# Performance work log

Hardware: AMD Instinct MI355X
Metric: run time of the kernel (lower is better)

Reference implementation:

```python
import jax, jax.numpy as jnp
import numpy as np

VOCAB = 50000
D = 256        # embedding_dim = nb_head * size_per_head
H = 8          # nb_head
DH = 32        # size_per_head
B = 8192
L = 64


def setup_inputs() -> dict:
    key = jax.random.key(0)
    ks = jax.random.split(key, 8)
    tokens = jax.random.randint(ks[0], (B, L), 0, VOCAB)
    scale = 0.02
    emb_table = jax.random.normal(ks[1], (VOCAB, D), dtype=jnp.float32) * scale
    WQ = jax.random.normal(ks[2], (D, D), dtype=jnp.float32) * scale
    WK = jax.random.normal(ks[3], (D, D), dtype=jnp.float32) * scale
    WV = jax.random.normal(ks[4], (D, D), dtype=jnp.float32) * scale
    WO = jax.random.normal(ks[5], (D, D), dtype=jnp.float32) * scale
    dense_w = jax.random.normal(ks[6], (D, 1), dtype=jnp.float32) * scale
    dense_b = jnp.zeros((1,), dtype=jnp.float32)
    return {"tokens": tokens, "emb_table": emb_table, "WQ": WQ, "WK": WK,
            "WV": WV, "WO": WO, "dense_w": dense_w, "dense_b": dense_b}


def _fastformer(x, WQ, WK, WV, WO):
    # x: [B, L, D]
    b, l, _ = x.shape
    Q = (x @ WQ).reshape(b, l, H, DH)
    K = (x @ WK).reshape(b, l, H, DH)
    V = (x @ WV).reshape(b, l, H, DH)
    global_q = jnp.mean(Q, axis=1, keepdims=True)   # [B,1,H,DH]
    global_k = jnp.mean(K, axis=1, keepdims=True)
    w = jnp.sum(global_q * K + global_k * Q, axis=-1)  # [B,L,H]
    w = jax.nn.softmax(w, axis=1)                       # softmax over seq
    context = (w[..., None] * V).reshape(b, l, D)
    return context @ WO


def reference(tokens, emb_table, WQ, WK, WV, WO, dense_w, dense_b):
    # NewsEncoder forward (inference: dropout = identity; masks computed but
    # unused by Fastformer.call, matching the original code).
    title_emb = emb_table[tokens]                       # [B,L,D]
    hidden = _fastformer(title_emb, WQ, WK, WV, WO)     # [B,L,D]
    scores = (hidden @ dense_w + dense_b)[..., 0]       # [B,L]
    attn = jax.nn.softmax(scores, axis=1)               # over seq
    news_vector = jnp.sum(hidden * attn[..., None], axis=1)  # [B,D]
    return news_vector
```

## Files before the change

### kernel.cpp

```cpp
#include <hip/hip_runtime.h>
#include <cstdint>


using f32x4  = __attribute__((ext_vector_type(4))) float;
using bf16x8 = __attribute__((ext_vector_type(8))) short;

__device__ __forceinline__ unsigned int pack2bf(float a, float b) {
  unsigned int ua = __builtin_bit_cast(unsigned int, a);
  unsigned int ub = __builtin_bit_cast(unsigned int, b);
  ua = (ua + 0x7fffu + ((ua >> 16) & 1u)) >> 16;
  ub = (ub + 0x7fffu + ((ub >> 16) & 1u)) >> 16;
  return ua | (ub << 16);
}
__device__ __forceinline__ unsigned short bf1(float a) {
  unsigned int ua = __builtin_bit_cast(unsigned int, a);
  ua = (ua + 0x7fffu + ((ua >> 16) & 1u)) >> 16;
  return (unsigned short)ua;
}
__device__ __forceinline__ float ubf(unsigned int u) {
  return __builtin_bit_cast(float, u << 16);
}
__device__ __forceinline__ void gload_lds16(const void* g, void* l) {
  __builtin_amdgcn_global_load_lds(
      (const __attribute__((address_space(1))) void*)g,
      (__attribute__((address_space(3))) void*)l, 16, 0, 0);
}

__global__ __launch_bounds__(256) void prep_all(const float* __restrict__ WQ,
                                                const float* __restrict__ WK,
                                                const float* __restrict__ WV,
                                                const float* __restrict__ WO,
                                                const float* __restrict__ dw,
                                                unsigned short* __restrict__ mbf,
                                                unsigned short* __restrict__ tkn,
                                                unsigned short* __restrict__ ptb) {
  const int t = threadIdx.x;
  const int bid = blockIdx.x;
  if (bid == 0) {
    __shared__ float wod[256];
    float acc = 0.f;
    for (int e = 0; e < 256; e += 4) {
      const float4 w4 = *(const float4*)(WO + (size_t)t * 256 + e);
      const float4 d4 = *(const float4*)(dw + e);
      acc += w4.x * d4.x + w4.y * d4.y + w4.z * d4.z + w4.w * d4.w;
    }
    wod[t] = acc;
    __syncthreads();
    for (int h = 0; h < 8; ++h) {
      float a = 0.f;
      for (int j = 0; j < 32; j += 4) {
        const float4 w4 = *(const float4*)(WV + (size_t)t * 256 + h * 32 + j);
        a += w4.x * wod[h*32+j] + w4.y * wod[h*32+j+1] + w4.z * wod[h*32+j+2] + w4.w * wod[h*32+j+3];
      }
      const float o = __shfl_xor(a, 1);
      if (!(t & 1)) ((unsigned int*)mbf)[h * 128 + (t >> 1)] = pack2bf(a, o);
    }
  } else if (bid <= 256) {
    __shared__ float ek[8][32], eq[8][32];
    const int n0 = (bid - 1) * 8;
    const int h  = n0 >> 8;
    {
      const int ei = t >> 5, j = t & 31;
      const int e = (n0 & 255) + ei;
      ek[ei][j] = WK[(size_t)e * 256 + h * 32 + j];
      eq[ei][j] = WQ[(size_t)e * 256 + h * 32 + j];
    }
    __syncthreads();
    float wqd[32], wkd[32];
#pragma unroll
    for (int j = 0; j < 32; j += 4) {
      *(float4*)(wqd + j) = *(const float4*)(WQ + (size_t)t * 256 + h * 32 + j);
      *(float4*)(wkd + j) = *(const float4*)(WK + (size_t)t * 256 + h * 32 + j);
    }
#pragma unroll
    for (int ei = 0; ei < 8; ++ei) {
      float a = 0.f;
#pragma unroll
      for (int j = 0; j < 32; ++j) a += wqd[j] * ek[ei][j] + wkd[j] * eq[ei][j];
      const float o = __shfl_xor(a, 1);
      if (!(t & 1)) ((unsigned int*)tkn)[(size_t)(n0 + ei) * 128 + (t >> 1)] = pack2bf(a, o);
    }
  } else {
    __shared__ float wvs[32][32];
    __shared__ float wos[32][256];
    const int pb = bid - 257;
    const int h = pb >> 3, d0 = (pb & 7) * 32;
    {
      const int dd = t >> 3, jq = (t & 7) * 4;
      *(float4*)(&wvs[dd][jq]) = *(const float4*)(WV + (size_t)(d0 + dd) * 256 + h * 32 + jq);
      const int c4 = (t & 63) * 4;
#pragma unroll
      for (int jj = 0; jj < 8; ++jj) {
        const int j = (t >> 6) * 8 + jj;
        *(float4*)(&wos[j][c4]) = *(const float4*)(WO + (size_t)(h * 32 + j) * 256 + c4);
      }
    }
    __syncthreads();
    const int n = t;
#pragma unroll 4
    for (int dd = 0; dd < 32; ++dd) {
      float a = 0.f;
#pragma unroll
      for (int j = 0; j < 32; ++j) a += wvs[dd][j] * wos[j][n];
      ptb[(size_t)n * 2048 + h * 256 + d0 + dd] = bf1(a);
    }
  }
}

__global__ __launch_bounds__(256) void ebf_kernel(const float4* __restrict__ emb4,
                                                  uint2* __restrict__ out2, int n) {
  for (int i = blockIdx.x * 256 + threadIdx.x; i < n; i += gridDim.x * 256) {
    const float4 v = emb4[i];
    uint2 pk;
    pk.x = pack2bf(v.x, v.y);
    pk.y = pack2bf(v.z, v.w);
    out2[i] = pk;
  }
}

__global__ __launch_bounds__(256) void xbar_kernel(const int* __restrict__ tokens,
                                                   const unsigned short* __restrict__ ebf,
                                                   unsigned short* __restrict__ xbf) {
  __shared__ int tok[64];
  __shared__ float part[8][256];
  const int b = blockIdx.x, t = threadIdx.x;
  if (t < 64) tok[t] = tokens[b * 64 + t];
  __syncthreads();
  const int rg = t >> 5;
  const int c16 = t & 31;
  const uint4* e4 = (const uint4*)ebf;
  float s[8] = {};
#pragma unroll
  for (int ri = 0; ri < 8; ++ri) {
    const uint4 u = e4[(size_t)tok[rg * 8 + ri] * 32 + c16];
    s[0] += ubf(u.x & 0xffffu); s[1] += ubf(u.x >> 16);
    s[2] += ubf(u.y & 0xffffu); s[3] += ubf(u.y >> 16);
    s[4] += ubf(u.z & 0xffffu); s[5] += ubf(u.z >> 16);
    s[6] += ubf(u.w & 0xffffu); s[7] += ubf(u.w >> 16);
  }
#pragma unroll
  for (int j = 0; j < 8; ++j) part[rg][c16 * 8 + j] = s[j];
  __syncthreads();
  float a = 0.f;
#pragma unroll
  for (int rg2 = 0; rg2 < 8; ++rg2) a += part[rg2][t];
  a *= (1.f / 64.f);
  const float o = __shfl_xor(a, 1);
  if (!(t & 1)) ((unsigned int*)xbf)[(size_t)b * 128 + (t >> 1)] = pack2bf(a, o);
}

__global__ __launch_bounds__(256) void cgemm(const unsigned short* __restrict__ xbf,
                                             const unsigned short* __restrict__ tkn,
                                             unsigned short* __restrict__ cbf) {
  __shared__ unsigned short As[64 * 264];
  const int t = threadIdx.x;
  const int m0 = blockIdx.x * 64, n0 = blockIdx.y * 64;
#pragma unroll
  for (int it = 0; it < 8; ++it) {
    const int idx = it * 256 + t;
    const int row = idx >> 5, c = idx & 31;
    const uint4 v = *(const uint4*)(xbf + (size_t)(m0 + row) * 256 + c * 8);
    *(uint4*)(As + row * 264 + c * 8) = v;
  }
  __syncthreads();
  const int wv = t >> 6, l = t & 63;
  const int g = l >> 4, r = l & 15;
#pragma unroll
  for (int nt = 0; nt < 4; ++nt) {
    const int n = n0 + nt * 16 + r;
    f32x4 acc = {0.f, 0.f, 0.f, 0.f};
#pragma unroll
    for (int kk = 0; kk < 8; ++kk) {
      const bf16x8 a  = *(const bf16x8*)(As + (16 * wv + r) * 264 + kk * 32 + g * 8);
      const bf16x8 bb = *(const bf16x8*)(tkn + (size_t)n * 256 + kk * 32 + g * 8);
      acc = __builtin_amdgcn_mfma_f32_16x16x32_bf16(a, bb, acc, 0, 0, 0);
    }
#pragma unroll
    for (int i = 0; i < 4; ++i)
      cbf[(size_t)(m0 + 16 * wv + g * 4 + i) * 2048 + n] = bf1(acc[i]);
  }
}

__global__ __launch_bounds__(256) void main_kernel(const int* __restrict__ tokens,
                                                   const unsigned short* __restrict__ ebf,
                                                   const unsigned short* __restrict__ mbf,
                                                   const float* __restrict__ dense_b,
                                                   unsigned short* __restrict__ cbf) {
  __shared__ unsigned short xl[64 * 256];
  __shared__ float wslds[64 * 17];
  __shared__ unsigned short cfT[16 * 80];
  const int t = threadIdx.x;
  const int b = blockIdx.x;
  const int wv = t >> 6, l = t & 63;
  const int g = l >> 4, r = l & 15;
  {
    unsigned int* cz = (unsigned int*)(cfT + 8 * 80);
    for (int z = t; z < 320; z += 256) cz[z] = 0u;
  }
  {
    const int ln = t & 63;
#pragma unroll
    for (int it = 0; it < 8; ++it) {
      const int R0 = it * 8 + wv * 2;
      const int R  = R0 + (ln >> 5);
      const int j  = ln & 31;
      const int tk = tokens[b * 64 + R];
      const int swzR = (R & 7) ^ (R >> 3);
      const unsigned short* src = ebf + (size_t)tk * 256 + ((j ^ swzR) << 3);
      gload_lds16(src, (void*)(xl + R0 * 256));
    }
  }
  __syncthreads();
  {
    const unsigned short* arow = xl + (16 * wv + r) * 256;
    const int sw = (r & 7) ^ ((2 * wv + (r >> 3)) & 7);
    const unsigned short* brow = (r < 8) ? (cbf + (size_t)b * 2048 + r * 256)
                                         : (mbf + (size_t)(r - 8) * 256);
    f32x4 acc = {0.f, 0.f, 0.f, 0.f};
#pragma unroll
    for (int kk = 0; kk < 8; ++kk) {
      const bf16x8 a  = *(const bf16x8*)(arow + (((kk * 4 + g) ^ sw) << 3));
      const bf16x8 bb = *(const bf16x8*)(brow + kk * 32 + g * 8);
      acc = __builtin_amdgcn_mfma_f32_16x16x32_bf16(a, bb, acc, 0, 0, 0);
    }
#pragma unroll
    for (int i = 0; i < 4; ++i)
      wslds[(16 * wv + g * 4 + i) * 17 + r] = acc[i];
  }
  __syncthreads();
  {
#pragma unroll
    for (int hh = 0; hh < 2; ++hh) {
      const int h = 2 * wv + hh;
      const float v = wslds[l * 17 + h];
      float mx = v;
#pragma unroll
      for (int sft = 32; sft; sft >>= 1) mx = fmaxf(mx, __shfl_xor(mx, sft));
      const float e = expf(v - mx);
      float sm = e;
#pragma unroll
      for (int sft = 32; sft; sft >>= 1) sm += __shfl_xor(sm, sft);
      wslds[l * 17 + h] = e / sm;
    }
  }
  __syncthreads();
  {
    float p[8], sv[8];
#pragma unroll
    for (int h = 0; h < 8; ++h) { p[h] = wslds[l*17 + h]; sv[h] = wslds[l*17 + 8 + h]; }
    float sc = dense_b[0];
#pragma unroll
    for (int h = 0; h < 8; ++h) sc += p[h] * sv[h];
    float mx = sc;
#pragma unroll
    for (int sft = 32; sft; sft >>= 1) mx = fmaxf(mx, __shfl_xor(mx, sft));
    const float e = expf(sc - mx);
    float sm = e;
#pragma unroll
    for (int sft = 32; sft; sft >>= 1) sm += __shfl_xor(sm, sft);
    const float attn = e / sm;
    float cc0, cc1;
    if      (wv == 0) { cc0 = attn * p[0]; cc1 = attn * p[1]; }
    else if (wv == 1) { cc0 = attn * p[2]; cc1 = attn * p[3]; }
    else if (wv == 2) { cc0 = attn * p[4]; cc1 = attn * p[5]; }
    else              { cc0 = attn * p[6]; cc1 = attn * p[7]; }
    cfT[(2 * wv) * 80 + l]     = bf1(cc0);
    cfT[(2 * wv + 1) * 80 + l] = bf1(cc1);
  }
  __syncthreads();
  {
    const bf16x8 a0 = *(const bf16x8*)(cfT + r * 80 + g * 8);
    const bf16x8 a1 = *(const bf16x8*)(cfT + r * 80 + 32 + g * 8);
    const short* xs = (const short*)xl;
#pragma unroll
    for (int nt = 0; nt < 4; ++nt) {
      const int d = wv * 64 + nt * 16 + r;
      short bv0[8], bv1[8];
#pragma unroll
      for (int j = 0; j < 8; ++j) {
        const int c0 = ((d >> 3) ^ j ^ g) << 3;
        bv0[j] = xs[(g * 8 + j) * 256 + (c0 | (d & 7))];
        const int c1 = ((d >> 3) ^ j ^ g ^ 4) << 3;
        bv1[j] = xs[(32 + g * 8 + j) * 256 + (c1 | (d & 7))];
      }
      f32x4 acc = {0.f, 0.f, 0.f, 0.f};
      acc = __builtin_amdgcn_mfma_f32_16x16x32_bf16(a0, *(const bf16x8*)bv0, acc, 0, 0, 0);
      acc = __builtin_amdgcn_mfma_f32_16x16x32_bf16(a1, *(const bf16x8*)bv1, acc, 0, 0, 0);
      if (g < 2) {
#pragma unroll
        for (int i = 0; i < 4; ++i) {
          const int h = g * 4 + i;
          cbf[(size_t)b * 2048 + h * 256 + d] = bf1(acc[i]);
        }
      }
    }
  }
}

__global__ __launch_bounds__(256) void pgemm(const unsigned short* __restrict__ cbf,
                                             const unsigned short* __restrict__ ptb,
                                             float* __restrict__ out) {
  __shared__ unsigned short As[32 * 264];
  const int t = threadIdx.x;
  const int m0 = blockIdx.x * 32, n0 = blockIdx.y * 64;
  const int wv = t >> 6, l = t & 63;
  const int g = l >> 4, r = l & 15;
  const int msub = wv & 1, nhalf = wv >> 1;
  f32x4 acc[2] = {};
  for (int kc = 0; kc < 8; ++kc) {
    __syncthreads();
#pragma unroll
    for (int it = 0; it < 4; ++it) {
      const int idx = it * 256 + t;
      const int row = idx >> 5, c = idx & 31;
      const uint4 v = *(const uint4*)(cbf + (size_t)(m0 + row) * 2048 + kc * 256 + c * 8);
      *(uint4*)(As + row * 264 + c * 8) = v;
    }
    __syncthreads();
#pragma unroll
    for (int kk = 0; kk < 8; ++kk) {
      const bf16x8 a = *(const bf16x8*)(As + (16 * msub + r) * 264 + kk * 32 + g * 8);
#pragma unroll
      for (int nt = 0; nt < 2; ++nt) {
        const int n = n0 + (nhalf * 2 + nt) * 16 + r;
        const bf16x8 bb = *(const bf16x8*)(ptb + (size_t)n * 2048 + kc * 256 + kk * 32 + g * 8);
        acc[nt] = __builtin_amdgcn_mfma_f32_16x16x32_bf16(a, bb, acc[nt], 0, 0, 0);
      }
    }
  }
#pragma unroll
  for (int nt = 0; nt < 2; ++nt) {
    const int n = n0 + (nhalf * 2 + nt) * 16 + r;
#pragma unroll
    for (int i = 0; i < 4; ++i)
      out[(size_t)(m0 + 16 * msub + g * 4 + i) * 256 + n] = acc[nt][i];
  }
}

extern "C" void kernel_launch(void* const* d_in, const int* in_sizes, int n_in,
                              void* d_out, int out_size, void* d_ws, size_t ws_size,
                              hipStream_t stream) {
  const int*   tokens = (const int*)d_in[0];
  const float* emb    = (const float*)d_in[1];
  const float* WQ     = (const float*)d_in[2];
  const float* WK     = (const float*)d_in[3];
  const float* WV     = (const float*)d_in[4];
  const float* WO     = (const float*)d_in[5];
  const float* dw     = (const float*)d_in[6];
  const float* db     = (const float*)d_in[7];
  float* out = (float*)d_out;

  unsigned short* base = (unsigned short*)d_ws;
  unsigned short* mbf  = base;
  unsigned short* xbf  = base + 2048;
  unsigned short* tkn  = xbf + (size_t)8192 * 256;
  unsigned short* cbf  = tkn + (size_t)2048 * 256;
  unsigned short* ebf  = cbf + (size_t)8192 * 2048;
  unsigned short* ptb  = ebf + (size_t)50000 * 256;

  const size_t need_bytes = (size_t)(2048 + 8192*256 + 2048*256 + 8192*2048
                                     + 50000*256 + 256*2048) * 2;
  if (ws_size < need_bytes) return;

  prep_all<<<dim3(321), dim3(256), 0, stream>>>(WQ, WK, WV, WO, dw, mbf, tkn, ptb);
  ebf_kernel<<<dim3(2048), dim3(256), 0, stream>>>((const float4*)emb, (uint2*)ebf,
                                                   50000 * 64);
  xbar_kernel<<<dim3(8192), dim3(256), 0, stream>>>(tokens, ebf, xbf);
  cgemm<<<dim3(128, 32), dim3(256), 0, stream>>>(xbf, tkn, cbf);
  main_kernel<<<dim3(8192), dim3(256), 0, stream>>>(tokens, ebf, mbf, db, cbf);
  pgemm<<<dim3(256, 4), dim3(256), 0, stream>>>(cbf, ptb, out);
}
```

Before: 261.5 us.

## Fuse embedding conversion into prep kernel and gather mean from 8-bit table

```diff
diff --git a/kernel.cpp b/kernel.cpp
--- a/kernel.cpp
+++ b/kernel.cpp
@@ -20,6 +20,13 @@
 __device__ __forceinline__ float ubf(unsigned int u) {
   return __builtin_bit_cast(float, u << 16);
 }
+__device__ __forceinline__ unsigned int b8(float f) {
+  const unsigned short u = __builtin_bit_cast(unsigned short, (_Float16)f);
+  return (unsigned int)((unsigned short)(u + 0x7Fu + ((u >> 8) & 1u)) >> 8);
+}
+__device__ __forceinline__ float d8(unsigned int v) {
+  return (float)__builtin_bit_cast(_Float16, (unsigned short)(v << 8));
+}
 __device__ __forceinline__ void gload_lds16(const void* g, void* l) {
   __builtin_amdgcn_global_load_lds(
       (const __attribute__((address_space(1))) void*)g,
@@ -31,9 +38,12 @@
                                                 const float* __restrict__ WV,
                                                 const float* __restrict__ WO,
                                                 const float* __restrict__ dw,
+                                                const float4* __restrict__ emb4,
                                                 unsigned short* __restrict__ mbf,
                                                 unsigned short* __restrict__ tkn,
-                                                unsigned short* __restrict__ ptb) {
+                                                unsigned short* __restrict__ ptb,
+                                                uint2* __restrict__ ebf2,
+                                                unsigned int* __restrict__ ebf8) {
   const int t = threadIdx.x;
   const int bid = blockIdx.x;
   if (bid == 0) {
@@ -80,7 +90,7 @@
       const float o = __shfl_xor(a, 1);
       if (!(t & 1)) ((unsigned int*)tkn)[(size_t)(n0 + ei) * 128 + (t >> 1)] = pack2bf(a, o);
     }
-  } else {
+  } else if (bid <= 320) {
     __shared__ float wvs[32][32];
     __shared__ float wos[32][256];
     const int pb = bid - 257;
@@ -104,42 +114,41 @@
       for (int j = 0; j < 32; ++j) a += wvs[dd][j] * wos[j][n];
       ptb[(size_t)n * 2048 + h * 256 + d0 + dd] = bf1(a);
     }
-  }
-}
-
-__global__ __launch_bounds__(256) void ebf_kernel(const float4* __restrict__ emb4,
-                                                  uint2* __restrict__ out2, int n) {
-  for (int i = blockIdx.x * 256 + threadIdx.x; i < n; i += gridDim.x * 256) {
-    const float4 v = emb4[i];
-    uint2 pk;
-    pk.x = pack2bf(v.x, v.y);
-    pk.y = pack2bf(v.z, v.w);
-    out2[i] = pk;
-  }
-}
-
-__global__ __launch_bounds__(256) void xbar_kernel(const int* __restrict__ tokens,
-                                                   const unsigned short* __restrict__ ebf,
-                                                   unsigned short* __restrict__ xbf) {
+  } else {
+    const int n = 50000 * 64;
+    for (int i = (bid - 321) * 256 + t; i < n; i += 2048 * 256) {
+      const float4 v = emb4[i];
+      uint2 pk;
+      pk.x = pack2bf(v.x, v.y);
+      pk.y = pack2bf(v.z, v.w);
+      ebf2[i] = pk;
+      ebf8[i] = b8(v.x) | (b8(v.y) << 8) | (b8(v.z) << 16) | (b8(v.w) << 24);
+    }
+  }
+}
+
+__global__ __launch_bounds__(256) void xbar8(const int* __restrict__ tokens,
+                                             const unsigned char* __restrict__ ebf8,
+                                             unsigned short* __restrict__ xbf) {
   __shared__ int tok[64];
   __shared__ float part[8][256];
   const int b = blockIdx.x, t = threadIdx.x;
   if (t < 64) tok[t] = tokens[b * 64 + t];
   __syncthreads();
   const int rg = t >> 5;
-  const int c16 = t & 31;
-  const uint4* e4 = (const uint4*)ebf;
+  const int c8 = t & 31;
+  const uint2* e8 = (const uint2*)ebf8;
   float s[8] = {};
 #pragma unroll
   for (int ri = 0; ri < 8; ++ri) {
-    const uint4 u = e4[(size_t)tok[rg * 8 + ri] * 32 + c16];
-    s[0] += ubf(u.x & 0xffffu); s[1] += ubf(u.x >> 16);
-    s[2] += ubf(u.y & 0xffffu); s[3] += ubf(u.y >> 16);
-    s[4] += ubf(u.z & 0xffffu); s[5] += ubf(u.z >> 16);
-    s[6] += ubf(u.w & 0xffffu); s[7] += ubf(u.w >> 16);
-  }
-#pragma unroll
-  for (int j = 0; j < 8; ++j) part[rg][c16 * 8 + j] = s[j];
+    const uint2 u = e8[(size_t)tok[rg * 8 + ri] * 32 + c8];
+    s[0] += d8(u.x & 0xffu);         s[1] += d8((u.x >> 8) & 0xffu);
+    s[2] += d8((u.x >> 16) & 0xffu); s[3] += d8(u.x >> 24);
+    s[4] += d8(u.y & 0xffu);         s[5] += d8((u.y >> 8) & 0xffu);
+    s[6] += d8((u.y >> 16) & 0xffu); s[7] += d8(u.y >> 24);
+  }
+#pragma unroll
+  for (int j = 0; j < 8; ++j) part[rg][c8 * 8 + j] = s[j];
   __syncthreads();
   float a = 0.f;
 #pragma unroll
@@ -357,15 +366,15 @@
   unsigned short* cbf  = tkn + (size_t)2048 * 256;
   unsigned short* ebf  = cbf + (size_t)8192 * 2048;
   unsigned short* ptb  = ebf + (size_t)50000 * 256;
+  unsigned char*  ebf8 = (unsigned char*)cbf;
 
   const size_t need_bytes = (size_t)(2048 + 8192*256 + 2048*256 + 8192*2048
                                      + 50000*256 + 256*2048) * 2;
   if (ws_size < need_bytes) return;
 
-  prep_all<<<dim3(321), dim3(256), 0, stream>>>(WQ, WK, WV, WO, dw, mbf, tkn, ptb);
-  ebf_kernel<<<dim3(2048), dim3(256), 0, stream>>>((const float4*)emb, (uint2*)ebf,
-                                                   50000 * 64);
-  xbar_kernel<<<dim3(8192), dim3(256), 0, stream>>>(tokens, ebf, xbf);
+  prep_all<<<dim3(2369), dim3(256), 0, stream>>>(WQ, WK, WV, WO, dw,
+      (const float4*)emb, mbf, tkn, ptb, (uint2*)ebf, (unsigned int*)ebf8);
+  xbar8<<<dim3(8192), dim3(256), 0, stream>>>(tokens, ebf8, xbf);
   cgemm<<<dim3(128, 32), dim3(256), 0, stream>>>(xbf, tkn, cbf);
   main_kernel<<<dim3(8192), dim3(256), 0, stream>>>(tokens, ebf, mbf, db, cbf);
   pgemm<<<dim3(256, 4), dim3(256), 0, stream>>>(cbf, ptb, out);
```

New measurement: 239.2 us. -8.5%, faster.
